# Performance work log

Measured on AMD Instinct MI355X. Metric: run time of the kernel, lower is better.

## Reference

```python
import jax, jax.numpy as jnp
import numpy as np

DIM = 1024
HEADS = 16
DIM_HEAD = 64
INNER = HEADS * DIM_HEAD  # 1024
MAX_LEN = 4096
BASE = 10000.0
EPS = 1.1920928955078125e-07  # torch.finfo(float32).eps (RMSNorm eps=None default)


def _rope_tables():
    t = np.arange(MAX_LEN, dtype=np.float32)
    inv_freq = 1.0 / (BASE ** (np.arange(0, DIM_HEAD, 2, dtype=np.float32) / DIM_HEAD))
    freqs = np.einsum('i,j->ij', t, inv_freq)          # [max_len, d/2]
    emb = np.concatenate([freqs, freqs], axis=-1)       # [max_len, d]
    return jnp.asarray(np.sin(emb)), jnp.asarray(np.cos(emb))


def setup_inputs() -> dict:
    key = jax.random.key(0)
    ks = jax.random.split(key, 5)
    x = jax.random.normal(ks[0], (2, 2048, DIM), dtype=jnp.float32)
    norm_w = jnp.ones((DIM,), dtype=jnp.float32)
    # store projection weights as [in, out] (transposed torch Linear weight)
    w_qkv = jax.random.normal(ks[1], (DIM, 3 * INNER), dtype=jnp.float32) * (DIM ** -0.5)
    w_o = jax.random.normal(ks[2], (INNER, DIM), dtype=jnp.float32) * (INNER ** -0.5)
    b_o = jax.random.normal(ks[3], (DIM,), dtype=jnp.float32) * 0.01
    sin, cos = _rope_tables()
    return {"x": x, "norm_w": norm_w, "w_qkv": w_qkv, "w_o": w_o, "b_o": b_o,
            "sin": sin, "cos": cos}


def _rotate_half(t):
    t1, t2 = jnp.split(t, 2, axis=-1)
    return jnp.concatenate([-t2, t1], axis=-1)


def _apply_rope(t, sin, cos):
    # t: [b, h, n, d]; sin/cos: [n, d]
    return t * cos + _rotate_half(t) * sin


def reference(x, norm_w, w_qkv, w_o, b_o, sin, cos):
    b, n, _ = x.shape
    # RMSNorm
    xn = x * jax.lax.rsqrt(jnp.mean(x * x, axis=-1, keepdims=True) + EPS) * norm_w
    # QKV projection
    qkv = xn @ w_qkv                                   # [b, n, 3*inner]
    q, k, v = jnp.split(qkv, 3, axis=-1)
    def to_heads(t):
        return t.reshape(b, n, HEADS, DIM_HEAD).transpose(0, 2, 1, 3)  # [b,h,n,d]
    q, k, v = to_heads(q), to_heads(k), to_heads(v)
    s, c = sin[:n], cos[:n]
    q = _apply_rope(q, s, c)
    k = _apply_rope(k, s, c)
    # causal SDPA
    scale = DIM_HEAD ** -0.5
    scores = jnp.einsum('bhqd,bhkd->bhqk', q, k) * scale
    causal = jnp.tril(jnp.ones((n, n), dtype=bool))
    scores = jnp.where(causal, scores, jnp.finfo(scores.dtype).min)
    attn = jax.nn.softmax(scores, axis=-1)
    out = jnp.einsum('bhqk,bhkd->bhqd', attn, v)
    out = out.transpose(0, 2, 1, 3).reshape(b, n, INNER)
    return out @ w_o + b_o
```

## Files before the change

kernel.cpp:

```cpp
#include <hip/hip_runtime.h>
#include <hip/hip_bf16.h>
#include <stdint.h>
#include <stddef.h>

#define NTOK   2048
#define NHEAD  16
#define DHEAD  64
#define DMODEL 1024
#define NROWS  4096
#define NQKV   3072
#define RMS_EPS 1.1920928955078125e-07f
#define QSCALE 0.1803368801111204f

typedef short bf16x8 __attribute__((ext_vector_type(8)));
typedef float f32x4  __attribute__((ext_vector_type(4)));
typedef unsigned short u16x4 __attribute__((ext_vector_type(4)));

__device__ __forceinline__ unsigned short f2b(float f) {
  unsigned u = __builtin_bit_cast(unsigned, f);
  return (unsigned short)((u + 0x7fffu + ((u >> 16) & 1u)) >> 16);
}

__device__ __forceinline__ unsigned pk2bf(float a, float b) {
  __hip_bfloat162 h = __float22bfloat162_rn(make_float2(a, b));
  unsigned u;
  __builtin_memcpy(&u, &h, 4);
  return u;
}

__device__ __forceinline__ void gl16(const void* g, void* l) {
  __builtin_amdgcn_global_load_lds((__attribute__((address_space(1))) void*)g,
                                   (__attribute__((address_space(3))) void*)l,
                                   16, 0, 0);
}

__global__ __launch_bounds__(256) void k_rmsnorm(const float* __restrict__ x,
                                                 const float* __restrict__ w,
                                                 unsigned short* __restrict__ xn) {
  int row = blockIdx.x;
  int t = threadIdx.x;
  float4 v = ((const float4*)(x + (size_t)row * DMODEL))[t];
  float ss = v.x * v.x + v.y * v.y + v.z * v.z + v.w * v.w;
#pragma unroll
  for (int m = 1; m < 64; m <<= 1) ss += __shfl_xor(ss, m, 64);
  __shared__ float red[4];
  if ((t & 63) == 0) red[t >> 6] = ss;
  __syncthreads();
  float tot = (red[0] + red[1]) + (red[2] + red[3]);
  float rs = rsqrtf(tot * (1.0f / DMODEL) + RMS_EPS);
  float4 wv = ((const float4*)w)[t];
  u16x4 o;
  o.x = f2b(v.x * rs * wv.x);
  o.y = f2b(v.y * rs * wv.y);
  o.z = f2b(v.z * rs * wv.z);
  o.w = f2b(v.w * rs * wv.w);
  *(u16x4*)(xn + (size_t)row * DMODEL + t * 4) = o;
}

__global__ __launch_bounds__(256) void k_transpose_bf16(const float* __restrict__ W,
                                                        unsigned short* __restrict__ Wt,
                                                        int K, int Nw) {
  __shared__ float tile[64][65];
  int bk = blockIdx.x * 64;
  int bn = blockIdx.y * 64;
  int t = threadIdx.x;
  int tr = t >> 4;
  int tc = (t & 15) * 4;
#pragma unroll
  for (int rr = 0; rr < 64; rr += 16) {
    float4 v = *(const float4*)&W[(size_t)(bk + tr + rr) * Nw + bn + tc];
    tile[tr + rr][tc + 0] = v.x;
    tile[tr + rr][tc + 1] = v.y;
    tile[tr + rr][tc + 2] = v.z;
    tile[tr + rr][tc + 3] = v.w;
  }
  __syncthreads();
#pragma unroll
  for (int rr = 0; rr < 64; rr += 16) {
    int n = bn + tr + rr;
    u16x4 o;
    o.x = f2b(tile[tc + 0][tr + rr]);
    o.y = f2b(tile[tc + 1][tr + rr]);
    o.z = f2b(tile[tc + 2][tr + rr]);
    o.w = f2b(tile[tc + 3][tr + rr]);
    *(u16x4*)&Wt[(size_t)n * K + bk + tc] = o;
  }
}

__global__ __launch_bounds__(256) void k_qkv_gemm(
    const unsigned short* __restrict__ A, const unsigned short* __restrict__ Bt,
    const float* __restrict__ sin_t, const float* __restrict__ cos_t,
    unsigned short* __restrict__ Qh, unsigned short* __restrict__ Kh,
    unsigned short* __restrict__ Vh) {
  __shared__ unsigned short As[2][128 * 32];
  __shared__ unsigned short Bs[2][128 * 32];
  int bm = blockIdx.x, bn = blockIdx.y;
  int t = threadIdx.x;
  int l = t & 63, w = t >> 6;
  int wr = w >> 1, wc = w & 1;
  int lr = l & 15, lg = l >> 4;
  f32x4 acc[4][4] = {};

  int srow = t >> 2;
  int scho = (t & 3) * 8;
  const unsigned short* Ag = A + (size_t)(bm * 128 + srow) * DMODEL + scho;
  const unsigned short* Bg = Bt + (size_t)(bn * 128 + srow) * DMODEL + scho;

  gl16(Ag, &As[0][t * 8]);
  gl16(Ag + 64 * DMODEL, &As[0][(t + 256) * 8]);
  gl16(Bg, &Bs[0][t * 8]);
  gl16(Bg + 64 * DMODEL, &Bs[0][(t + 256) * 8]);
  __syncthreads();

  for (int i = 0; i < 32; i++) {
    int cur = i & 1, nxt = cur ^ 1;
    if (i < 31) {
      int k1 = (i + 1) * 32;
      gl16(Ag + k1, &As[nxt][t * 8]);
      gl16(Ag + k1 + 64 * DMODEL, &As[nxt][(t + 256) * 8]);
      gl16(Bg + k1, &Bs[nxt][t * 8]);
      gl16(Bg + k1 + 64 * DMODEL, &Bs[nxt][(t + 256) * 8]);
    }
    bf16x8 af[4], bfr[4];
#pragma unroll
    for (int ii = 0; ii < 4; ii++)
      af[ii] = *(const bf16x8*)&As[cur][(wr * 64 + ii * 16 + lr) * 32 + lg * 8];
#pragma unroll
    for (int jj = 0; jj < 4; jj++)
      bfr[jj] = *(const bf16x8*)&Bs[cur][(wc * 64 + jj * 16 + lr) * 32 + lg * 8];
#pragma unroll
    for (int ii = 0; ii < 4; ii++)
#pragma unroll
      for (int jj = 0; jj < 4; jj++)
        acc[ii][jj] = __builtin_amdgcn_mfma_f32_16x16x32_bf16(af[ii], bfr[jj], acc[ii][jj], 0, 0, 0);
    __syncthreads();
  }

  int nc0 = bn * 128 + wc * 64;
  int which = nc0 >> 10;
  int h = (nc0 & 1023) >> 6;
#pragma unroll
  for (int i = 0; i < 4; i++) {
#pragma unroll
    for (int r = 0; r < 4; r++) {
      int m = bm * 128 + wr * 64 + i * 16 + lg * 4 + r;
      int b = m >> 11;
      int n = m & (NTOK - 1);
      size_t obase = ((size_t)(b * NHEAD + h) * NTOK + n) * DHEAD;
      if (which == 2) {
#pragma unroll
        for (int j = 0; j < 4; j++) Vh[obase + j * 16 + lr] = f2b(acc[i][j][r]);
      } else {
        unsigned short* dst = which ? Kh : Qh;
        float qs = which ? 1.0f : QSCALE;
#pragma unroll
        for (int j = 0; j < 2; j++) {
          int d = j * 16 + lr;
          float t1 = acc[i][j][r];
          float t2 = acc[i][j + 2][r];
          float c1 = cos_t[n * DHEAD + d],      s1 = sin_t[n * DHEAD + d];
          float c2 = cos_t[n * DHEAD + d + 32], s2 = sin_t[n * DHEAD + d + 32];
          dst[obase + d]      = f2b((t1 * c1 - t2 * s1) * qs);
          dst[obase + d + 32] = f2b((t2 * c2 + t1 * s2) * qs);
        }
      }
    }
  }
}

__global__ __launch_bounds__(256, 4) void k_attn(
    const unsigned short* __restrict__ Qh, const unsigned short* __restrict__ Kh,
    const unsigned short* __restrict__ Vh, unsigned short* __restrict__ AO) {
  int bh = blockIdx.x;
  int j  = blockIdx.y;
  int m8 = j & 7, k8 = j >> 3;
  int qt = (k8 == 0) ? 31 - m8 : (k8 == 1) ? m8 : (k8 == 2) ? 23 - m8 : 8 + m8;
  int t = threadIdx.x;
  int l = t & 63, w = t >> 6;
  int lr = l & 15, lg = l >> 4;

  __shared__ unsigned short Ks[2][64 * 64];
  __shared__ unsigned short Vt[2][64 * 64];
  __shared__ unsigned short Ps[4][16 * 64];

  const unsigned short* Qb = Qh + (size_t)bh * NTOK * DHEAD;
  const unsigned short* Kb = Kh + (size_t)bh * NTOK * DHEAD;
  const unsigned short* Vb = Vh + (size_t)bh * NTOK * DHEAD;

  int qrow = qt * 64 + w * 16 + lr;
  bf16x8 aq0 = *(const bf16x8*)&Qb[(size_t)qrow * DHEAD + lg * 8];
  bf16x8 aq1 = *(const bf16x8*)&Qb[(size_t)qrow * DHEAD + 32 + lg * 8];

  f32x4 accO[4] = {};
  float mrow = -1e38f;
  float lsum = 0.f;

  int srow = t >> 3;
  int spc  = t & 7;
  int vr0  = (t >> 3) * 2;

  gl16(Kb + (size_t)srow * DHEAD + (spc ^ (srow & 7)) * 8, &Ks[0][t * 8]);
  gl16(Kb + (size_t)(srow + 32) * DHEAD + (spc ^ ((srow + 32) & 7)) * 8, &Ks[0][(t + 256) * 8]);
  {
    bf16x8 v0 = *(const bf16x8*)&Vb[(size_t)vr0 * DHEAD + spc * 8];
    bf16x8 v1 = *(const bf16x8*)&Vb[(size_t)(vr0 + 1) * DHEAD + spc * 8];
#pragma unroll
    for (int jj = 0; jj < 8; jj++) {
      int d = spc * 8 + jj;
      int sw = ((d & 7) ^ ((d >> 3) & 7)) << 4;
      unsigned pk = (unsigned)(unsigned short)v0[jj] | ((unsigned)(unsigned short)v1[jj] << 16);
      *(unsigned*)((char*)Vt[0] + d * 128 + ((vr0 * 2) ^ sw)) = pk;
    }
  }
  __syncthreads();

  for (int kt = 0; kt <= qt; ++kt) {
    int cur = kt & 1, nxt = cur ^ 1;
    int kv0 = kt * 64;
    bool notlast = (kt < qt);

    bf16x8 pv0, pv1;
    if (notlast) {
      int kvn = kv0 + 64;
      gl16(Kb + (size_t)(kvn + srow) * DHEAD + (spc ^ (srow & 7)) * 8, &Ks[nxt][t * 8]);
      gl16(Kb + (size_t)(kvn + srow + 32) * DHEAD + (spc ^ ((srow + 32) & 7)) * 8,
           &Ks[nxt][(t + 256) * 8]);
      pv0 = *(const bf16x8*)&Vb[(size_t)(kvn + vr0) * DHEAD + spc * 8];
      pv1 = *(const bf16x8*)&Vb[(size_t)(kvn + vr0 + 1) * DHEAD + spc * 8];
    }

    f32x4 s[4];
#pragma unroll
    for (int nf = 0; nf < 4; nf++) {
      int krow = nf * 16 + lr;
      const char* kbase = (const char*)Ks[cur] + krow * 128;
      bf16x8 bk0 = *(const bf16x8*)(kbase + ((lg * 16) ^ ((krow & 7) << 4)));
      bf16x8 bk1 = *(const bf16x8*)(kbase + ((lg * 16 + 64) ^ ((krow & 7) << 4)));
      f32x4 z = {};
      z = __builtin_amdgcn_mfma_f32_16x16x32_bf16(bk0, aq0, z, 0, 0, 0);
      s[nf] = __builtin_amdgcn_mfma_f32_16x16x32_bf16(bk1, aq1, z, 0, 0, 0);
    }

    if (kt == qt) {
      int qr = qt * 64 + w * 16 + lr;
#pragma unroll
      for (int nf = 0; nf < 4; nf++)
#pragma unroll
        for (int r = 0; r < 4; r++)
          if (kv0 + nf * 16 + lg * 4 + r > qr) s[nf][r] = -1e30f;
    }

    float t1m = fmaxf(fmaxf(s[0][0], s[0][1]), s[0][2]);
    float t2m = fmaxf(fmaxf(s[0][3], s[1][0]), s[1][1]);
    float t3m = fmaxf(fmaxf(s[1][2], s[1][3]), s[2][0]);
    float t4m = fmaxf(fmaxf(s[2][1], s[2][2]), s[2][3]);
    float t5m = fmaxf(fmaxf(s[3][0], s[3][1]), s[3][2]);
    float pm = fmaxf(fmaxf(fmaxf(t1m, t2m), t3m), fmaxf(fmaxf(t4m, t5m), s[3][3]));
    pm = fmaxf(pm, __shfl_xor(pm, 16, 64));
    pm = fmaxf(pm, __shfl_xor(pm, 32, 64));
    if (__any(pm > mrow + 8.0f)) {
      float mnew = fmaxf(mrow, pm);
      float corr = exp2f(mrow - mnew);
      mrow = mnew;
      lsum *= corr;
      float c0 = __shfl(corr, lg * 4 + 0, 64);
      float c1 = __shfl(corr, lg * 4 + 1, 64);
      float c2 = __shfl(corr, lg * 4 + 2, 64);
      float c3 = __shfl(corr, lg * 4 + 3, 64);
#pragma unroll
      for (int df = 0; df < 4; df++) {
        accO[df][0] *= c0; accO[df][1] *= c1;
        accO[df][2] *= c2; accO[df][3] *= c3;
      }
    }
    {
      float m = mrow;
      float sum = 0.f;
      char* pw = (char*)Ps[w] + lr * 128;
      int sw = (lr & 7) << 4;
#pragma unroll
      for (int nf = 0; nf < 4; nf++) {
        float p0 = exp2f(s[nf][0] - m);
        float p1 = exp2f(s[nf][1] - m);
        float p2 = exp2f(s[nf][2] - m);
        float p3 = exp2f(s[nf][3] - m);
        sum += (p0 + p1) + (p2 + p3);
        unsigned w0 = pk2bf(p0, p1);
        unsigned w1 = pk2bf(p2, p3);
        *(uint64_t*)(pw + ((nf * 32 + lg * 8) ^ sw)) = (uint64_t)w0 | ((uint64_t)w1 << 32);
      }
      sum += __shfl_xor(sum, 16, 64);
      sum += __shfl_xor(sum, 32, 64);
      lsum += sum;
    }

#pragma unroll
    for (int ks = 0; ks < 2; ks++) {
      const char* pb = (const char*)Ps[w] + lr * 128;
      bf16x8 ap = *(const bf16x8*)(pb + ((lg * 16 + ks * 64) ^ ((lr & 7) << 4)));
#pragma unroll
      for (int df = 0; df < 4; df++) {
        int col = df * 16 + lr;
        int sw = ((col & 7) ^ ((col >> 3) & 7)) << 4;
        bf16x8 bv = *(const bf16x8*)((const char*)Vt[cur] + col * 128 + ((lg * 16 + ks * 64) ^ sw));
        accO[df] = __builtin_amdgcn_mfma_f32_16x16x32_bf16(ap, bv, accO[df], 0, 0, 0);
      }
    }

    if (notlast) {
#pragma unroll
      for (int jj = 0; jj < 8; jj++) {
        int d = spc * 8 + jj;
        int sw = ((d & 7) ^ ((d >> 3) & 7)) << 4;
        unsigned pk = (unsigned)(unsigned short)pv0[jj] | ((unsigned)(unsigned short)pv1[jj] << 16);
        *(unsigned*)((char*)Vt[nxt] + d * 128 + ((vr0 * 2) ^ sw)) = pk;
      }
    }
    __syncthreads();
  }

  int b = bh >> 4, h = bh & 15;
  float li = 1.0f / lsum;
  float l0 = __shfl(li, lg * 4 + 0, 64);
  float l1 = __shfl(li, lg * 4 + 1, 64);
  float l2 = __shfl(li, lg * 4 + 2, 64);
  float l3 = __shfl(li, lg * 4 + 3, 64);
  int qbase = qt * 64 + w * 16;
#pragma unroll
  for (int df = 0; df < 4; df++) {
    int d = df * 16 + lr;
    size_t ob = ((size_t)(b * NTOK + qbase + lg * 4)) * DMODEL + h * DHEAD + d;
    AO[ob + 0 * DMODEL] = f2b(accO[df][0] * l0);
    AO[ob + 1 * DMODEL] = f2b(accO[df][1] * l1);
    AO[ob + 2 * DMODEL] = f2b(accO[df][2] * l2);
    AO[ob + 3 * DMODEL] = f2b(accO[df][3] * l3);
  }
}

__global__ __launch_bounds__(256) void k_out_gemm(
    const unsigned short* __restrict__ A, const unsigned short* __restrict__ Bt,
    const float* __restrict__ bias, float* __restrict__ out) {
  __shared__ unsigned short As[2][128 * 32];
  __shared__ unsigned short Bs[2][64 * 32];
  int bm = blockIdx.x, bn = blockIdx.y;
  int t = threadIdx.x;
  int l = t & 63, w = t >> 6;
  int wr = w >> 1, wc = w & 1;
  int lr = l & 15, lg = l >> 4;
  f32x4 acc[4][2] = {};

  int srow = t >> 2;
  int scho = (t & 3) * 8;
  const unsigned short* Ag = A + (size_t)(bm * 128 + srow) * DMODEL + scho;
  const unsigned short* Bg = Bt + (size_t)(bn * 64 + srow) * DMODEL + scho;

  gl16(Ag, &As[0][t * 8]);
  gl16(Ag + 64 * DMODEL, &As[0][(t + 256) * 8]);
  if (srow < 64) gl16(Bg, &Bs[0][t * 8]);
  __syncthreads();

  for (int i = 0; i < 32; i++) {
    int cur = i & 1, nxt = cur ^ 1;
    if (i < 31) {
      int k1 = (i + 1) * 32;
      gl16(Ag + k1, &As[nxt][t * 8]);
      gl16(Ag + k1 + 64 * DMODEL, &As[nxt][(t + 256) * 8]);
      if (srow < 64) gl16(Bg + k1, &Bs[nxt][t * 8]);
    }
    bf16x8 af[4], bfr[2];
#pragma unroll
    for (int ii = 0; ii < 4; ii++)
      af[ii] = *(const bf16x8*)&As[cur][(wr * 64 + ii * 16 + lr) * 32 + lg * 8];
#pragma unroll
    for (int jj = 0; jj < 2; jj++)
      bfr[jj] = *(const bf16x8*)&Bs[cur][(wc * 32 + jj * 16 + lr) * 32 + lg * 8];
#pragma unroll
    for (int ii = 0; ii < 4; ii++)
#pragma unroll
      for (int jj = 0; jj < 2; jj++)
        acc[ii][jj] = __builtin_amdgcn_mfma_f32_16x16x32_bf16(af[ii], bfr[jj], acc[ii][jj], 0, 0, 0);
    __syncthreads();
  }
  int nc0 = bn * 64 + wc * 32;
#pragma unroll
  for (int i = 0; i < 4; i++)
#pragma unroll
    for (int r = 0; r < 4; r++) {
      int m = bm * 128 + wr * 64 + i * 16 + lg * 4 + r;
      float* orow = out + (size_t)m * DMODEL;
#pragma unroll
      for (int j = 0; j < 2; j++) {
        int col = nc0 + j * 16 + lr;
        orow[col] = acc[i][j][r] + bias[col];
      }
    }
}

extern "C" void kernel_launch(void* const* d_in, const int* in_sizes, int n_in,
                              void* d_out, int out_size, void* d_ws, size_t ws_size,
                              hipStream_t stream) {
  const float* x      = (const float*)d_in[0];
  const float* norm_w = (const float*)d_in[1];
  const float* w_qkv  = (const float*)d_in[2];
  const float* w_o    = (const float*)d_in[3];
  const float* b_o    = (const float*)d_in[4];
  const float* sin_t  = (const float*)d_in[5];
  const float* cos_t  = (const float*)d_in[6];
  float* out = (float*)d_out;

  char* ws = (char*)d_ws;
  unsigned short* xn    = (unsigned short*)(ws + (0u << 20));
  unsigned short* wqkvT = (unsigned short*)(ws + (8u << 20));
  unsigned short* woT   = (unsigned short*)(ws + (14u << 20));
  unsigned short* Qh    = (unsigned short*)(ws + (16u << 20));
  unsigned short* Kh    = (unsigned short*)(ws + (24u << 20));
  unsigned short* Vh    = (unsigned short*)(ws + (32u << 20));
  unsigned short* AO    = (unsigned short*)(ws + (40u << 20));

  hipLaunchKernelGGL(k_rmsnorm, dim3(NROWS), dim3(256), 0, stream, x, norm_w, xn);
  hipLaunchKernelGGL(k_transpose_bf16, dim3(16, 48), dim3(256), 0, stream, w_qkv, wqkvT, DMODEL, NQKV);
  hipLaunchKernelGGL(k_transpose_bf16, dim3(16, 16), dim3(256), 0, stream, w_o, woT, DMODEL, DMODEL);
  hipLaunchKernelGGL(k_qkv_gemm, dim3(32, 24), dim3(256), 0, stream, xn, wqkvT, sin_t, cos_t, Qh, Kh, Vh);
  hipLaunchKernelGGL(k_attn, dim3(32, 32), dim3(256), 0, stream, Qh, Kh, Vh, AO);
  hipLaunchKernelGGL(k_out_gemm, dim3(32, 16), dim3(256), 0, stream, AO, woT, b_o, out);
}
```

Measured before the change: 120.5 us.

## Split long causal attention rows into two KV halves with a merge kernel

The attention launch changes from 32 query tiles per head to 48 work slots. Query tiles 16-31 have their KV range split into two partial blocks, chosen so each slot does a similar amount of work and the tail imbalance of the causal grid shrinks. Partial blocks write unnormalised bf16 outputs plus row max and sum to workspace (reusing the xn/wqkvT region), and a new merge kernel combines them into AO. This adds an extra launch, extra global traffic, and bf16 rounding of the partial outputs before the merge.

```diff
diff --git a/kernel.cpp b/kernel.cpp
--- a/kernel.cpp
+++ b/kernel.cpp
@@ -15,6 +15,7 @@
 typedef short bf16x8 __attribute__((ext_vector_type(8)));
 typedef float f32x4  __attribute__((ext_vector_type(4)));
 typedef unsigned short u16x4 __attribute__((ext_vector_type(4)));
+typedef unsigned short u16x8 __attribute__((ext_vector_type(8)));
 
 __device__ __forceinline__ unsigned short f2b(float f) {
   unsigned u = __builtin_bit_cast(unsigned, f);
@@ -168,13 +169,30 @@
   }
 }
 
+#define SL(q, a, b) ((q) | ((a) << 6) | ((b) << 12))
+__constant__ int SLOTS[48] = {
+  SL(31,0,16), SL(31,16,32), SL(30,15,31), SL(15,0,16),
+  SL(30,0,15), SL(29,0,15),  SL(29,15,30), SL(28,14,29), SL(14,0,15),
+  SL(28,0,14), SL(27,0,14),  SL(27,14,28), SL(26,13,27), SL(13,0,14),
+  SL(26,0,13), SL(25,0,13),  SL(25,13,26), SL(24,12,25), SL(12,0,13),
+  SL(24,0,12), SL(23,0,12),  SL(23,12,24), SL(22,11,23), SL(11,0,12),
+  SL(22,0,11), SL(21,0,11),  SL(21,11,22), SL(20,10,21), SL(10,0,11),
+  SL(20,0,10), SL(19,0,10),  SL(19,10,20), SL(18,9,19),  SL(9,0,10),
+  SL(18,0,9),  SL(17,0,9),   SL(17,9,18),  SL(16,8,17),  SL(8,0,9),
+  SL(16,0,8),  SL(7,0,8),    SL(6,0,7),    SL(5,0,6),    SL(4,0,5),
+  SL(3,0,4),   SL(2,0,3),    SL(1,0,2),    SL(0,0,1)
+};
+
 __global__ __launch_bounds__(256, 4) void k_attn(
     const unsigned short* __restrict__ Qh, const unsigned short* __restrict__ Kh,
-    const unsigned short* __restrict__ Vh, unsigned short* __restrict__ AO) {
+    const unsigned short* __restrict__ Vh, unsigned short* __restrict__ AO,
+    unsigned short* __restrict__ Opart, float* __restrict__ Mpart,
+    float* __restrict__ Lpart) {
   int bh = blockIdx.x;
-  int j  = blockIdx.y;
-  int m8 = j & 7, k8 = j >> 3;
-  int qt = (k8 == 0) ? 31 - m8 : (k8 == 1) ? m8 : (k8 == 2) ? 23 - m8 : 8 + m8;
+  int sv = SLOTS[blockIdx.y];
+  int qt = sv & 63, kt0 = (sv >> 6) & 63, kt1 = sv >> 12;
+  bool partial = (kt0 != 0) || (kt1 != qt + 1);
+  int half = (kt0 != 0) ? 1 : 0;
   int t = threadIdx.x;
   int l = t & 63, w = t >> 6;
   int lr = l & 15, lg = l >> 4;
@@ -199,11 +217,13 @@
   int spc  = t & 7;
   int vr0  = (t >> 3) * 2;
 
-  gl16(Kb + (size_t)srow * DHEAD + (spc ^ (srow & 7)) * 8, &Ks[0][t * 8]);
-  gl16(Kb + (size_t)(srow + 32) * DHEAD + (spc ^ ((srow + 32) & 7)) * 8, &Ks[0][(t + 256) * 8]);
   {
-    bf16x8 v0 = *(const bf16x8*)&Vb[(size_t)vr0 * DHEAD + spc * 8];
-    bf16x8 v1 = *(const bf16x8*)&Vb[(size_t)(vr0 + 1) * DHEAD + spc * 8];
+    int kv0 = kt0 * 64;
+    gl16(Kb + (size_t)(kv0 + srow) * DHEAD + (spc ^ (srow & 7)) * 8, &Ks[0][t * 8]);
+    gl16(Kb + (size_t)(kv0 + srow + 32) * DHEAD + (spc ^ ((srow + 32) & 7)) * 8,
+         &Ks[0][(t + 256) * 8]);
+    bf16x8 v0 = *(const bf16x8*)&Vb[(size_t)(kv0 + vr0) * DHEAD + spc * 8];
+    bf16x8 v1 = *(const bf16x8*)&Vb[(size_t)(kv0 + vr0 + 1) * DHEAD + spc * 8];
 #pragma unroll
     for (int jj = 0; jj < 8; jj++) {
       int d = spc * 8 + jj;
@@ -214,10 +234,10 @@
   }
   __syncthreads();
 
-  for (int kt = 0; kt <= qt; ++kt) {
-    int cur = kt & 1, nxt = cur ^ 1;
+  for (int kt = kt0; kt < kt1; ++kt) {
+    int cur = (kt - kt0) & 1, nxt = cur ^ 1;
     int kv0 = kt * 64;
-    bool notlast = (kt < qt);
+    bool notlast = (kt + 1 < kt1);
 
     bf16x8 pv0, pv1;
     if (notlast) {
@@ -319,21 +339,69 @@
     __syncthreads();
   }
 
+  if (partial) {
+    int pbase = (((bh << 4) + (qt - 16)) << 1) + half;
+    if (lg == 0) {
+      Mpart[pbase * 64 + w * 16 + lr] = mrow;
+      Lpart[pbase * 64 + w * 16 + lr] = lsum;
+    }
+    unsigned short* Od = Opart + (size_t)pbase * 4096;
+#pragma unroll
+    for (int df = 0; df < 4; df++)
+#pragma unroll
+      for (int r = 0; r < 4; r++)
+        Od[(w * 16 + lg * 4 + r) * 64 + df * 16 + lr] = f2b(accO[df][r]);
+  } else {
+    int b = bh >> 4, h = bh & 15;
+    float li = 1.0f / lsum;
+    float l0 = __shfl(li, lg * 4 + 0, 64);
+    float l1 = __shfl(li, lg * 4 + 1, 64);
+    float l2 = __shfl(li, lg * 4 + 2, 64);
+    float l3 = __shfl(li, lg * 4 + 3, 64);
+    int qbase = qt * 64 + w * 16;
+#pragma unroll
+    for (int df = 0; df < 4; df++) {
+      int d = df * 16 + lr;
+      size_t ob = ((size_t)(b * NTOK + qbase + lg * 4)) * DMODEL + h * DHEAD + d;
+      AO[ob + 0 * DMODEL] = f2b(accO[df][0] * l0);
+      AO[ob + 1 * DMODEL] = f2b(accO[df][1] * l1);
+      AO[ob + 2 * DMODEL] = f2b(accO[df][2] * l2);
+      AO[ob + 3 * DMODEL] = f2b(accO[df][3] * l3);
+    }
+  }
+}
+
+__global__ __launch_bounds__(256) void k_merge(const unsigned short* __restrict__ Opart,
+                                               const float* __restrict__ Mpart,
+                                               const float* __restrict__ Lpart,
+                                               unsigned short* __restrict__ AO) {
+  int bh = blockIdx.x, qq = blockIdx.y;
+  int t = threadIdx.x;
+  int row = t >> 2, d0 = (t & 3) << 4;
+  int p0 = ((bh << 4) + qq) << 1;
+  float m1 = Mpart[p0 * 64 + row],       l1 = Lpart[p0 * 64 + row];
+  float m2 = Mpart[(p0 + 1) * 64 + row], l2 = Lpart[(p0 + 1) * 64 + row];
+  float mm = fmaxf(m1, m2);
+  float s1 = exp2f(m1 - mm), s2 = exp2f(m2 - mm);
+  float li = 1.0f / (l1 * s1 + l2 * s2);
+  float a1 = s1 * li, a2 = s2 * li;
+  const unsigned short* O1 = Opart + (size_t)p0 * 4096 + row * 64 + d0;
+  const unsigned short* O2 = O1 + 4096;
+  int qt = 16 + qq;
   int b = bh >> 4, h = bh & 15;
-  float li = 1.0f / lsum;
-  float l0 = __shfl(li, lg * 4 + 0, 64);
-  float l1 = __shfl(li, lg * 4 + 1, 64);
-  float l2 = __shfl(li, lg * 4 + 2, 64);
-  float l3 = __shfl(li, lg * 4 + 3, 64);
-  int qbase = qt * 64 + w * 16;
-#pragma unroll
-  for (int df = 0; df < 4; df++) {
-    int d = df * 16 + lr;
-    size_t ob = ((size_t)(b * NTOK + qbase + lg * 4)) * DMODEL + h * DHEAD + d;
-    AO[ob + 0 * DMODEL] = f2b(accO[df][0] * l0);
-    AO[ob + 1 * DMODEL] = f2b(accO[df][1] * l1);
-    AO[ob + 2 * DMODEL] = f2b(accO[df][2] * l2);
-    AO[ob + 3 * DMODEL] = f2b(accO[df][3] * l3);
+  unsigned short* dst = AO + ((size_t)(b * NTOK + qt * 64 + row)) * DMODEL + h * DHEAD + d0;
+#pragma unroll
+  for (int c = 0; c < 2; c++) {
+    u16x8 v1 = *(const u16x8*)(O1 + c * 8);
+    u16x8 v2 = *(const u16x8*)(O2 + c * 8);
+    u16x8 o;
+#pragma unroll
+    for (int e = 0; e < 8; e++) {
+      float f1 = __builtin_bit_cast(float, (unsigned)v1[e] << 16);
+      float g1 = __builtin_bit_cast(float, (unsigned)v2[e] << 16);
+      o[e] = f2b(f1 * a1 + g1 * a2);
+    }
+    *(u16x8*)(dst + c * 8) = o;
   }
 }
 
@@ -416,11 +484,15 @@
   unsigned short* Kh    = (unsigned short*)(ws + (24u << 20));
   unsigned short* Vh    = (unsigned short*)(ws + (32u << 20));
   unsigned short* AO    = (unsigned short*)(ws + (40u << 20));
+  unsigned short* Opart = (unsigned short*)(ws + (0u << 20));
+  float*          Mpart = (float*)(ws + (8u << 20));
+  float*          Lpart = (float*)(ws + (8u << 20) + (1u << 18));
 
   hipLaunchKernelGGL(k_rmsnorm, dim3(NROWS), dim3(256), 0, stream, x, norm_w, xn);
   hipLaunchKernelGGL(k_transpose_bf16, dim3(16, 48), dim3(256), 0, stream, w_qkv, wqkvT, DMODEL, NQKV);
   hipLaunchKernelGGL(k_transpose_bf16, dim3(16, 16), dim3(256), 0, stream, w_o, woT, DMODEL, DMODEL);
   hipLaunchKernelGGL(k_qkv_gemm, dim3(32, 24), dim3(256), 0, stream, xn, wqkvT, sin_t, cos_t, Qh, Kh, Vh);
-  hipLaunchKernelGGL(k_attn, dim3(32, 32), dim3(256), 0, stream, Qh, Kh, Vh, AO);
+  hipLaunchKernelGGL(k_attn, dim3(32, 48), dim3(256), 0, stream, Qh, Kh, Vh, AO, Opart, Mpart, Lpart);
+  hipLaunchKernelGGL(k_merge, dim3(32, 16), dim3(256), 0, stream, Opart, Mpart, Lpart, AO);
   hipLaunchKernelGGL(k_out_gemm, dim3(32, 16), dim3(256), 0, stream, AO, woT, b_o, out);
 }
```

New measurement: 120.0 us. No clear change (-0.4%).
